# Performance work log

Measured on AMD Instinct MI355X. Metric: run time of the kernel, lower is better.

The kernel has to match this reference:

```python
import jax, jax.numpy as jnp
import numpy as np

N = 524288
D = 256
NUM_SEGMENTS = 8192


def setup_inputs() -> dict:
    key = jax.random.key(0)
    k = jax.random.split(key, 6)
    s = 1.0 / np.sqrt(D)
    s2 = 1.0 / np.sqrt(2 * D)
    return {
        "x": jax.random.normal(k[0], (N, D), dtype=jnp.float32),
        "batch_index": jnp.sort(jax.random.randint(k[1], (N,), 0, NUM_SEGMENTS, dtype=jnp.int32)),
        "W1": jax.random.uniform(k[2], (D, D), jnp.float32, -s, s),
        "b1": jax.random.uniform(k[3], (D,), jnp.float32, -s, s),
        "Wp": jax.random.uniform(k[4], (D, 2 * D), jnp.float32, -s2, s2),
        "bp": jax.random.uniform(k[5], (D,), jnp.float32, -s2, s2),
    }


def reference(x, batch_index, W1, b1, Wp, bp):
    # prepool linear: [N, D]
    h = x @ W1.T + b1
    # scatter-mean over groups
    seg_sum = jax.ops.segment_sum(h, batch_index, num_segments=NUM_SEGMENTS)
    counts = jax.ops.segment_sum(jnp.ones((h.shape[0],), h.dtype), batch_index, num_segments=NUM_SEGMENTS)
    xmean = seg_sum / jnp.maximum(counts, 1.0)[:, None]
    # scatter-max over groups (empty segments -> 0, matching torch_scatter default fill; they are never gathered)
    xmax = jax.ops.segment_max(h, batch_index, num_segments=NUM_SEGMENTS)
    xmax = jnp.where(jnp.isfinite(xmax), xmax, jnp.zeros_like(xmax))
    # meanmax concat -> proj -> gather back to entities
    xpool = jnp.concatenate([xmean, xmax], axis=1)  # [B, 2D]
    out = xpool @ Wp.T + bp  # [B, D]
    return out[batch_index]  # [N, D]
```

## Files before the change

### kernel.cpp

```cpp
#include <hip/hip_runtime.h>

#define NROWS 524288
#define DIM 256
#define NSEG 8192
#define SPB 8
#define SEGS3 8

typedef __attribute__((ext_vector_type(8))) short bf16x8;
typedef __attribute__((ext_vector_type(4))) float f32x4;

__device__ __forceinline__ short f2bf(float f) {
  union { float f; unsigned u; } a; a.f = f;
  unsigned r = a.u + 0x7fffu + ((a.u >> 16) & 1u);
  return (short)(r >> 16);
}

__global__ void seg_start_kernel(const int* __restrict__ bi, int* __restrict__ ss) {
  int s = blockIdx.x * blockDim.x + threadIdx.x;
  if (s > NSEG) return;
  int lo = 0, hi = NROWS;
  while (lo < hi) { int mid = (lo + hi) >> 1; if (bi[mid] < s) lo = mid + 1; else hi = mid; }
  ss[s] = lo;
}

__global__ __launch_bounds__(256, 2) void gemm_pool_kernel(
    const float* __restrict__ x, const float* __restrict__ W1,
    const float* __restrict__ b1, const int* __restrict__ ss,
    float* __restrict__ xpool) {
  __shared__ short x_lds[2][16 * 264];

  const int tid  = threadIdx.x;
  const int wave = tid >> 6, lane = tid & 63;
  const int quad = lane >> 4, l16 = lane & 15;

  const int s0i = blockIdx.x * SPB;
  const int r0 = ss[s0i];
  const int r1 = ss[s0i + SPB];
  if (r0 >= r1) return;

  bf16x8 bfr[4][8];
  #pragma unroll
  for (int tt = 0; tt < 4; ++tt) {
    const int col = wave * 64 + tt * 16 + l16;
    #pragma unroll
    for (int ks = 0; ks < 8; ++ks) {
      const float* p = W1 + (size_t)col * DIM + ks * 32 + quad * 8;
      f32x4 w0 = *(const f32x4*)p;
      f32x4 w1 = *(const f32x4*)(p + 4);
      bf16x8 f;
      f[0]=f2bf(w0[0]); f[1]=f2bf(w0[1]); f[2]=f2bf(w0[2]); f[3]=f2bf(w0[3]);
      f[4]=f2bf(w1[0]); f[5]=f2bf(w1[1]); f[6]=f2bf(w1[2]); f[7]=f2bf(w1[3]);
      bfr[tt][ks] = f;
    }
  }
  const float b1f = b1[wave * 64 + quad * 16 + l16];

  const int srow = tid >> 4;
  const int scol = (tid & 15) * 16;

  {
    const int row = r0 + srow;
    if (row < r1) {
      const float* xp = x + (size_t)row * DIM + scol;
      f32x4 v0 = *(const f32x4*)xp;
      f32x4 v1 = *(const f32x4*)(xp + 4);
      f32x4 v2 = *(const f32x4*)(xp + 8);
      f32x4 v3 = *(const f32x4*)(xp + 12);
      bf16x8 a0, a1;
      a0[0]=f2bf(v0[0]); a0[1]=f2bf(v0[1]); a0[2]=f2bf(v0[2]); a0[3]=f2bf(v0[3]);
      a0[4]=f2bf(v1[0]); a0[5]=f2bf(v1[1]); a0[6]=f2bf(v1[2]); a0[7]=f2bf(v1[3]);
      a1[0]=f2bf(v2[0]); a1[1]=f2bf(v2[1]); a1[2]=f2bf(v2[2]); a1[3]=f2bf(v2[3]);
      a1[4]=f2bf(v3[0]); a1[5]=f2bf(v3[1]); a1[6]=f2bf(v3[2]); a1[7]=f2bf(v3[3]);
      *(bf16x8*)&x_lds[0][srow * 264 + scol] = a0;
      *(bf16x8*)&x_lds[0][srow * 264 + scol + 8] = a1;
    }
  }
  __syncthreads();

  int idx = 0;
  int seg_lo = r0;
  int seg_hi = ss[s0i + 1];
  while (seg_hi == seg_lo) { ++idx; seg_lo = seg_hi; seg_hi = ss[s0i + idx + 1]; }

  float ssum[4] = {0.f, 0.f, 0.f, 0.f};
  float smax[4] = {-3.0e38f, -3.0e38f, -3.0e38f, -3.0e38f};

  const int nch = (r1 - r0 + 15) >> 4;
  for (int c = 0; c < nch; ++c) {
    const int base = r0 + c * 16;
    int nr = r1 - base; if (nr > 16) nr = 16;

    f32x4 v0, v1, v2, v3;
    const int prow = base + 16 + srow;
    const bool pf = (prow < r1);
    if (pf) {
      const float* xp = x + (size_t)prow * DIM + scol;
      v0 = *(const f32x4*)xp;
      v1 = *(const f32x4*)(xp + 4);
      v2 = *(const f32x4*)(xp + 8);
      v3 = *(const f32x4*)(xp + 12);
    }

    const short* xb = x_lds[c & 1];
    f32x4 acc[4] = {{0.f,0.f,0.f,0.f},{0.f,0.f,0.f,0.f},{0.f,0.f,0.f,0.f},{0.f,0.f,0.f,0.f}};
    #pragma unroll
    for (int ks = 0; ks < 8; ++ks) {
      bf16x8 a = *(const bf16x8*)&xb[l16 * 264 + ks * 32 + quad * 8];
      acc[0] = __builtin_amdgcn_mfma_f32_16x16x32_bf16(a, bfr[0][ks], acc[0], 0, 0, 0);
      acc[1] = __builtin_amdgcn_mfma_f32_16x16x32_bf16(a, bfr[1][ks], acc[1], 0, 0, 0);
      acc[2] = __builtin_amdgcn_mfma_f32_16x16x32_bf16(a, bfr[2][ks], acc[2], 0, 0, 0);
      acc[3] = __builtin_amdgcn_mfma_f32_16x16x32_bf16(a, bfr[3][ks], acc[3], 0, 0, 0);
    }

    int r = 0;
    while (r < nr) {
      int e = seg_hi - base; if (e > nr) e = nr;
      if (r == 0 && e == 16) {
        #pragma unroll
        for (int tt = 0; tt < 4; ++tt) {
          ssum[tt] += (acc[tt][0] + acc[tt][1]) + (acc[tt][2] + acc[tt][3]);
          smax[tt] = fmaxf(smax[tt], fmaxf(fmaxf(acc[tt][0], acc[tt][1]),
                                           fmaxf(acc[tt][2], acc[tt][3])));
        }
      } else {
        #pragma unroll
        for (int tt = 0; tt < 4; ++tt) {
          #pragma unroll
          for (int j = 0; j < 4; ++j) {
            const int row = (quad << 2) + j;
            const bool in = (row >= r) && (row < e);
            ssum[tt] += in ? acc[tt][j] : 0.f;
            smax[tt] = in ? fmaxf(smax[tt], acc[tt][j]) : smax[tt];
          }
        }
      }
      if (base + e == seg_hi) {
        float c0 = ssum[0], c1 = ssum[1], c2 = ssum[2], c3 = ssum[3];
        c0 += __shfl_xor(c0, 16); c0 += __shfl_xor(c0, 32);
        c1 += __shfl_xor(c1, 16); c1 += __shfl_xor(c1, 32);
        c2 += __shfl_xor(c2, 16); c2 += __shfl_xor(c2, 32);
        c3 += __shfl_xor(c3, 16); c3 += __shfl_xor(c3, 32);
        float m0 = smax[0], m1 = smax[1], m2 = smax[2], m3 = smax[3];
        m0 = fmaxf(m0, __shfl_xor(m0, 16)); m0 = fmaxf(m0, __shfl_xor(m0, 32));
        m1 = fmaxf(m1, __shfl_xor(m1, 16)); m1 = fmaxf(m1, __shfl_xor(m1, 32));
        m2 = fmaxf(m2, __shfl_xor(m2, 16)); m2 = fmaxf(m2, __shfl_xor(m2, 32));
        m3 = fmaxf(m3, __shfl_xor(m3, 16)); m3 = fmaxf(m3, __shfl_xor(m3, 32));
        const float fs = (quad & 2) ? ((quad & 1) ? c3 : c2) : ((quad & 1) ? c1 : c0);
        const float fm = (quad & 2) ? ((quad & 1) ? m3 : m2) : ((quad & 1) ? m1 : m0);
        const float inv = 1.f / (float)(seg_hi - seg_lo);
        const int col = wave * 64 + quad * 16 + l16;
        xpool[(size_t)(s0i + idx) * 512 + col]       = fs * inv + b1f;
        xpool[(size_t)(s0i + idx) * 512 + 256 + col] = fm + b1f;
        ssum[0]=0.f; ssum[1]=0.f; ssum[2]=0.f; ssum[3]=0.f;
        smax[0]=-3.0e38f; smax[1]=-3.0e38f; smax[2]=-3.0e38f; smax[3]=-3.0e38f;
        if (base + e < r1) {
          do { ++idx; seg_lo = seg_hi; seg_hi = ss[s0i + idx + 1]; } while (seg_hi == seg_lo);
        }
      }
      r = e;
    }

    if (pf) {
      bf16x8 a0, a1;
      a0[0]=f2bf(v0[0]); a0[1]=f2bf(v0[1]); a0[2]=f2bf(v0[2]); a0[3]=f2bf(v0[3]);
      a0[4]=f2bf(v1[0]); a0[5]=f2bf(v1[1]); a0[6]=f2bf(v1[2]); a0[7]=f2bf(v1[3]);
      a1[0]=f2bf(v2[0]); a1[1]=f2bf(v2[1]); a1[2]=f2bf(v2[2]); a1[3]=f2bf(v2[3]);
      a1[4]=f2bf(v3[0]); a1[5]=f2bf(v3[1]); a1[6]=f2bf(v3[2]); a1[7]=f2bf(v3[3]);
      short* dst = &x_lds[(c + 1) & 1][srow * 264 + scol];
      *(bf16x8*)dst = a0;
      *(bf16x8*)(dst + 8) = a1;
    }
    __syncthreads();
  }
}

__global__ __launch_bounds__(256) void proj_kernel(
    const float* __restrict__ xpool, const float* __restrict__ Wp,
    const float* __restrict__ bp, float* __restrict__ out_pool) {
  __shared__ float xp_lds[SEGS3 * 512];
  const int tid = threadIdx.x;
  const size_t s0 = (size_t)blockIdx.x * SEGS3;
  for (int i = tid; i < SEGS3 * 128; i += 256)
    *(f32x4*)&xp_lds[i * 4] = *(const f32x4*)&xpool[s0 * 512 + (size_t)i * 4];
  __syncthreads();
  float acc[SEGS3];
  #pragma unroll
  for (int s = 0; s < SEGS3; ++s) acc[s] = 0.f;
  for (int k0 = 0; k0 < 512; k0 += 4) {
    f32x4 wp = *(const f32x4*)&Wp[(size_t)tid * 512 + k0];
    #pragma unroll
    for (int s = 0; s < SEGS3; ++s) {
      f32x4 xv = *(const f32x4*)&xp_lds[s * 512 + k0];
      acc[s] += xv[0]*wp[0] + xv[1]*wp[1] + xv[2]*wp[2] + xv[3]*wp[3];
    }
  }
  const float b = bp[tid];
  #pragma unroll
  for (int s = 0; s < SEGS3; ++s)
    out_pool[(s0 + s) * 256 + tid] = acc[s] + b;
}

__global__ __launch_bounds__(256) void gather_kernel(const int* __restrict__ bi,
                              const float* __restrict__ out_pool,
                              float* __restrict__ out) {
  const size_t idx = (size_t)blockIdx.x * blockDim.x + threadIdx.x;
  const int n  = (int)(idx >> 6);
  const int c4 = (int)(idx & 63);
  const int s = bi[n];
  f32x4 v = *(const f32x4*)&out_pool[(size_t)s * 256 + c4 * 4];
  *(f32x4*)&out[(size_t)n * 256 + (size_t)c4 * 4] = v;
}

extern "C" void kernel_launch(void* const* d_in, const int* in_sizes, int n_in,
                              void* d_out, int out_size, void* d_ws, size_t ws_size,
                              hipStream_t stream) {
  const float* x  = (const float*)d_in[0];
  const int*   bi = (const int*)d_in[1];
  const float* W1 = (const float*)d_in[2];
  const float* b1 = (const float*)d_in[3];
  const float* Wp = (const float*)d_in[4];
  const float* bp = (const float*)d_in[5];
  float* out = (float*)d_out;

  char* ws = (char*)d_ws;
  int*   ss       = (int*)ws;
  float* xpool    = (float*)(ws + 64 * 1024);
  float* out_pool = (float*)(ws + 64 * 1024 + (size_t)NSEG * 512 * 4);

  seg_start_kernel<<<(NSEG + 256) / 256, 256, 0, stream>>>(bi, ss);
  gemm_pool_kernel<<<NSEG / SPB, 256, 0, stream>>>(x, W1, b1, ss, xpool);
  proj_kernel<<<NSEG / SEGS3, 256, 0, stream>>>(xpool, Wp, bp, out_pool);
  gather_kernel<<<(size_t)NROWS * (DIM / 4) / 256, 256, 0, stream>>>(bi, out_pool, out);
}
```

Before: 1.074 ms.

## Deepen x prefetch pipeline, use nontemporal loads, gather by segment

The fused GEMM+pool kernel now keeps two chunks of x loads in flight through alternating register sets, so global loads run two chunks ahead of compute, and it reads x with nontemporal loads. The gather kernel is reorganised to one block per segment that reads its pooled row once and writes it to all member rows with nontemporal stores, removing the per-element batch_index reads. This costs more registers in the GEMM kernel, which may lower occupancy, and the gather may see imbalance across segments of different sizes.

```diff
diff --git a/kernel.cpp b/kernel.cpp
--- a/kernel.cpp
+++ b/kernel.cpp
@@ -58,25 +58,6 @@
   const int srow = tid >> 4;
   const int scol = (tid & 15) * 16;
 
-  {
-    const int row = r0 + srow;
-    if (row < r1) {
-      const float* xp = x + (size_t)row * DIM + scol;
-      f32x4 v0 = *(const f32x4*)xp;
-      f32x4 v1 = *(const f32x4*)(xp + 4);
-      f32x4 v2 = *(const f32x4*)(xp + 8);
-      f32x4 v3 = *(const f32x4*)(xp + 12);
-      bf16x8 a0, a1;
-      a0[0]=f2bf(v0[0]); a0[1]=f2bf(v0[1]); a0[2]=f2bf(v0[2]); a0[3]=f2bf(v0[3]);
-      a0[4]=f2bf(v1[0]); a0[5]=f2bf(v1[1]); a0[6]=f2bf(v1[2]); a0[7]=f2bf(v1[3]);
-      a1[0]=f2bf(v2[0]); a1[1]=f2bf(v2[1]); a1[2]=f2bf(v2[2]); a1[3]=f2bf(v2[3]);
-      a1[4]=f2bf(v3[0]); a1[5]=f2bf(v3[1]); a1[6]=f2bf(v3[2]); a1[7]=f2bf(v3[3]);
-      *(bf16x8*)&x_lds[0][srow * 264 + scol] = a0;
-      *(bf16x8*)&x_lds[0][srow * 264 + scol + 8] = a1;
-    }
-  }
-  __syncthreads();
-
   int idx = 0;
   int seg_lo = r0;
   int seg_hi = ss[s0i + 1];
@@ -84,25 +65,36 @@
 
   float ssum[4] = {0.f, 0.f, 0.f, 0.f};
   float smax[4] = {-3.0e38f, -3.0e38f, -3.0e38f, -3.0e38f};
-
-  const int nch = (r1 - r0 + 15) >> 4;
-  for (int c = 0; c < nch; ++c) {
+  f32x4 acc[4];
+
+  auto issue_loads = [&](int prow, f32x4& v0, f32x4& v1, f32x4& v2, f32x4& v3) -> bool {
+    bool pf = (prow < r1);
+    if (pf) {
+      const f32x4* xp = (const f32x4*)(x + (size_t)prow * DIM + scol);
+      v0 = __builtin_nontemporal_load(xp);
+      v1 = __builtin_nontemporal_load(xp + 1);
+      v2 = __builtin_nontemporal_load(xp + 2);
+      v3 = __builtin_nontemporal_load(xp + 3);
+    }
+    return pf;
+  };
+  auto stage_write = [&](int buf, const f32x4& v0, const f32x4& v1,
+                         const f32x4& v2, const f32x4& v3) {
+    bf16x8 a0, a1;
+    a0[0]=f2bf(v0[0]); a0[1]=f2bf(v0[1]); a0[2]=f2bf(v0[2]); a0[3]=f2bf(v0[3]);
+    a0[4]=f2bf(v1[0]); a0[5]=f2bf(v1[1]); a0[6]=f2bf(v1[2]); a0[7]=f2bf(v1[3]);
+    a1[0]=f2bf(v2[0]); a1[1]=f2bf(v2[1]); a1[2]=f2bf(v2[2]); a1[3]=f2bf(v2[3]);
+    a1[4]=f2bf(v3[0]); a1[5]=f2bf(v3[1]); a1[6]=f2bf(v3[2]); a1[7]=f2bf(v3[3]);
+    short* dst = &x_lds[buf][srow * 264 + scol];
+    *(bf16x8*)dst = a0;
+    *(bf16x8*)(dst + 8) = a1;
+  };
+  auto compute_chunk = [&](int c) {
     const int base = r0 + c * 16;
     int nr = r1 - base; if (nr > 16) nr = 16;
-
-    f32x4 v0, v1, v2, v3;
-    const int prow = base + 16 + srow;
-    const bool pf = (prow < r1);
-    if (pf) {
-      const float* xp = x + (size_t)prow * DIM + scol;
-      v0 = *(const f32x4*)xp;
-      v1 = *(const f32x4*)(xp + 4);
-      v2 = *(const f32x4*)(xp + 8);
-      v3 = *(const f32x4*)(xp + 12);
-    }
-
     const short* xb = x_lds[c & 1];
-    f32x4 acc[4] = {{0.f,0.f,0.f,0.f},{0.f,0.f,0.f,0.f},{0.f,0.f,0.f,0.f},{0.f,0.f,0.f,0.f}};
+    acc[0] = (f32x4){0.f,0.f,0.f,0.f}; acc[1] = (f32x4){0.f,0.f,0.f,0.f};
+    acc[2] = (f32x4){0.f,0.f,0.f,0.f}; acc[3] = (f32x4){0.f,0.f,0.f,0.f};
     #pragma unroll
     for (int ks = 0; ks < 8; ++ks) {
       bf16x8 a = *(const bf16x8*)&xb[l16 * 264 + ks * 32 + quad * 8];
@@ -111,7 +103,6 @@
       acc[2] = __builtin_amdgcn_mfma_f32_16x16x32_bf16(a, bfr[2][ks], acc[2], 0, 0, 0);
       acc[3] = __builtin_amdgcn_mfma_f32_16x16x32_bf16(a, bfr[3][ks], acc[3], 0, 0, 0);
     }
-
     int r = 0;
     while (r < nr) {
       int e = seg_hi - base; if (e > nr) e = nr;
@@ -159,17 +150,28 @@
       }
       r = e;
     }
-
-    if (pf) {
-      bf16x8 a0, a1;
-      a0[0]=f2bf(v0[0]); a0[1]=f2bf(v0[1]); a0[2]=f2bf(v0[2]); a0[3]=f2bf(v0[3]);
-      a0[4]=f2bf(v1[0]); a0[5]=f2bf(v1[1]); a0[6]=f2bf(v1[2]); a0[7]=f2bf(v1[3]);
-      a1[0]=f2bf(v2[0]); a1[1]=f2bf(v2[1]); a1[2]=f2bf(v2[2]); a1[3]=f2bf(v2[3]);
-      a1[4]=f2bf(v3[0]); a1[5]=f2bf(v3[1]); a1[6]=f2bf(v3[2]); a1[7]=f2bf(v3[3]);
-      short* dst = &x_lds[(c + 1) & 1][srow * 264 + scol];
-      *(bf16x8*)dst = a0;
-      *(bf16x8*)(dst + 8) = a1;
-    }
+  };
+
+  const int nch = (r1 - r0 + 15) >> 4;
+
+  f32x4 a0v, a1v, a2v, a3v, b0v, b1v_, b2v, b3v;
+  bool pfa = false, pfb = false;
+  {
+    bool p0 = issue_loads(r0 + srow, b0v, b1v_, b2v, b3v);
+    if (p0) stage_write(0, b0v, b1v_, b2v, b3v);
+  }
+  pfa = issue_loads(r0 + 16 + srow, a0v, a1v, a2v, a3v);
+  __syncthreads();
+
+  for (int c = 0; c < nch; c += 2) {
+    pfb = issue_loads(r0 + (c + 2) * 16 + srow, b0v, b1v_, b2v, b3v);
+    compute_chunk(c);
+    if (pfa) stage_write((c + 1) & 1, a0v, a1v, a2v, a3v);
+    __syncthreads();
+    if (c + 1 >= nch) break;
+    pfa = issue_loads(r0 + (c + 3) * 16 + srow, a0v, a1v, a2v, a3v);
+    compute_chunk(c + 1);
+    if (pfb) stage_write(c & 1, b0v, b1v_, b2v, b3v);
     __syncthreads();
   }
 }
@@ -200,15 +202,18 @@
     out_pool[(s0 + s) * 256 + tid] = acc[s] + b;
 }
 
-__global__ __launch_bounds__(256) void gather_kernel(const int* __restrict__ bi,
-                              const float* __restrict__ out_pool,
-                              float* __restrict__ out) {
-  const size_t idx = (size_t)blockIdx.x * blockDim.x + threadIdx.x;
-  const int n  = (int)(idx >> 6);
-  const int c4 = (int)(idx & 63);
-  const int s = bi[n];
-  f32x4 v = *(const f32x4*)&out_pool[(size_t)s * 256 + c4 * 4];
-  *(f32x4*)&out[(size_t)n * 256 + (size_t)c4 * 4] = v;
+__global__ __launch_bounds__(256) void gather_kernel(
+    const int* __restrict__ ss, const float* __restrict__ out_pool,
+    float* __restrict__ out) {
+  const int s = blockIdx.x;
+  const int lo = ss[s], hi = ss[s + 1];
+  if (lo >= hi) return;
+  const int tid = threadIdx.x;
+  const int rofs = tid >> 6;
+  const int c4 = tid & 63;
+  const f32x4 v = *(const f32x4*)&out_pool[(size_t)s * 256 + (size_t)c4 * 4];
+  for (int n = lo + rofs; n < hi; n += 4)
+    __builtin_nontemporal_store(v, (f32x4*)&out[(size_t)n * 256 + (size_t)c4 * 4]);
 }
 
 extern "C" void kernel_launch(void* const* d_in, const int* in_sizes, int n_in,
@@ -230,5 +235,5 @@
   seg_start_kernel<<<(NSEG + 256) / 256, 256, 0, stream>>>(bi, ss);
   gemm_pool_kernel<<<NSEG / SPB, 256, 0, stream>>>(x, W1, b1, ss, xpool);
   proj_kernel<<<NSEG / SEGS3, 256, 0, stream>>>(xpool, Wp, bp, out_pool);
-  gather_kernel<<<(size_t)NROWS * (DIM / 4) / 256, 256, 0, stream>>>(bi, out_pool, out);
-}
+  gather_kernel<<<NSEG, 256, 0, stream>>>(ss, out_pool, out);
+}
```

Result: no change. 1.061 ms (-1.2%).
